# Performance work log

Hardware: AMD Instinct MI355X
Metric: run time of the kernel (lower is better)

## Reference

```python
import jax, jax.numpy as jnp
import numpy as np

EPS = 1e-5  # torch LayerNorm default


def setup_inputs() -> dict:
    key = jax.random.key(0)
    ks = jax.random.split(key, 6)
    B, C, H, W, D = 8, 128, 64, 64, 32
    x = jax.random.normal(ks[0], (B, C, H, W), dtype=jnp.float32)
    gamma = jnp.ones((C,), dtype=jnp.float32)
    beta = jnp.zeros((C,), dtype=jnp.float32)
    Wq = jax.random.normal(ks[1], (D, C), dtype=jnp.float32) * 0.02
    Wk = jax.random.normal(ks[2], (D, C), dtype=jnp.float32) * 0.02
    Wv = jax.random.normal(ks[3], (C, C), dtype=jnp.float32) * 0.02
    Wo = jax.random.normal(ks[4], (C, C), dtype=jnp.float32) * (1.0 / np.sqrt(C))
    bo = jnp.zeros((C,), dtype=jnp.float32)
    return {"x": x, "gamma": gamma, "beta": beta, "Wq": Wq, "Wk": Wk,
            "Wv": Wv, "Wo": Wo, "bo": bo}


def reference(x, gamma, beta, Wq, Wk, Wv, Wo, bo):
    B, C, H, W = x.shape
    # LayerNorm over channel dim (applied in NHWC in the original)
    xn = x.transpose(0, 2, 3, 1)                       # [B,H,W,C]
    mu = xn.mean(-1, keepdims=True)
    var = ((xn - mu) ** 2).mean(-1, keepdims=True)
    xn = (xn - mu) * jax.lax.rsqrt(var + EPS) * gamma + beta
    xn = xn.transpose(0, 3, 1, 2)                      # [B,C,H,W]
    # 1x1-conv projections == channel matmuls
    q = jnp.einsum('dc,bchw->bdhw', Wq, xn)
    k = jnp.einsum('dc,bchw->bdhw', Wk, xn)
    v = jnp.einsum('oc,bchw->bohw', Wv, xn)
    # full spatial attention: scores [B,H,W,H,W], softmax over key positions
    scores = jnp.einsum('bchw,bcxy->bhwxy', q, k)
    scores = scores.reshape(B, H, W, H * W)
    attn = jax.nn.softmax(scores, axis=-1).reshape(B, H, W, H, W)
    out = jnp.einsum('bhwxy,bcxy->bchw', attn, v)
    out = jnp.einsum('oc,bchw->bohw', Wo, out) + bo[None, :, None, None]
    return out + x
```

## Files before the change

kernel.cpp:

```cpp
#include <hip/hip_runtime.h>


#define NB 8
#define CCH 128
#define NTOK 4096
#define DQK 32
#define KT 64

typedef __attribute__((ext_vector_type(8))) short bf16x8;
typedef __attribute__((ext_vector_type(4))) float f32x4;
typedef unsigned short u16;
typedef unsigned int u32;

static __device__ __forceinline__ f32x4 mfma16(bf16x8 a, bf16x8 b, f32x4 c) {
  return __builtin_amdgcn_mfma_f32_16x16x32_bf16(a, b, c, 0, 0, 0);
}
static __device__ __forceinline__ u16 f2bf(float f) {
  union { float f; u32 u; } cv; cv.f = f;
  u32 u = cv.u;
  u += 0x7fffu + ((u >> 16) & 1u);
  return (u16)(u >> 16);
}
static __device__ __forceinline__ float bf2f(u16 v) {
  union { u32 u; float f; } cv; cv.u = ((u32)v) << 16;
  return cv.f;
}
static __device__ __forceinline__ u32 cvtpk(float lo, float hi) {
  u32 d;
  asm("v_cvt_pk_bf16_f32 %0, %1, %2" : "=v"(d) : "v"(lo), "v"(hi));
  return d;
}
static __device__ __forceinline__ void gload16(const void* g, void* l) {
  __builtin_amdgcn_global_load_lds(
      (const __attribute__((address_space(1))) void*)g,
      (__attribute__((address_space(3))) void*)l, 16, 0, 0);
}

__global__ __launch_bounds__(256) void wconv_kernel(
    const float* __restrict__ Wq, const float* __restrict__ Wk,
    const float* __restrict__ Wv, const float* __restrict__ Wo,
    u16* __restrict__ wcomb) {
  int idx = blockIdx.x * 256 + threadIdx.x;
  int r = idx >> 7;
  float v;
  if (r < 32)        v = Wq[idx];
  else if (r < 64)   v = Wk[idx - 4096];
  else if (r < 192)  v = Wv[idx - 8192];
  else               v = Wo[idx - 24576];
  wcomb[idx] = f2bf(v);
}

__global__ __launch_bounds__(256) void lnqkv_kernel(
    const float* __restrict__ x, const float* __restrict__ gamma,
    const float* __restrict__ beta, const u16* __restrict__ wcomb,
    u16* __restrict__ Qg, u16* __restrict__ Kg, u16* __restrict__ Vt) {
  __shared__ float tile[128][64];
  __shared__ float red[2][4][64];
  __shared__ u16   xt[64][130];
  int t = threadIdx.x;
  int lane = t & 63, cq = t >> 6;
  int b = blockIdx.x >> 6;
  int posb = (blockIdx.x & 63) << 6;
  const float* xb = x + ((size_t)b * CCH) * NTOK + posb;
  for (int i = 0; i < 32; ++i) {
    int c = cq * 32 + i;
    tile[c][lane] = xb[(size_t)c * NTOK + lane];
  }
  __syncthreads();
  float s = 0.f, s2 = 0.f;
  for (int i = 0; i < 32; ++i) {
    float v = tile[cq * 32 + i][lane];
    s += v; s2 += v * v;
  }
  red[0][cq][lane] = s; red[1][cq][lane] = s2;
  __syncthreads();
  float mu  = (red[0][0][lane] + red[0][1][lane] + red[0][2][lane] + red[0][3][lane]) * (1.f / 128.f);
  float ex2 = (red[1][0][lane] + red[1][1][lane] + red[1][2][lane] + red[1][3][lane]) * (1.f / 128.f);
  float rstd = rsqrtf(ex2 - mu * mu + 1e-5f);
  for (int i = 0; i < 32; ++i) {
    int c = cq * 32 + i;
    float v = (tile[c][lane] - mu) * rstd * gamma[c] + beta[c];
    xt[lane][c] = f2bf(v);
  }
  __syncthreads();
  int w = t >> 6, row16 = lane & 15, kgrp = lane >> 4;
  bf16x8 af[4];
  for (int ks = 0; ks < 4; ++ks)
    af[ks] = *(const bf16x8*)&xt[w * 16 + row16][ks * 32 + kgrp * 8];
  f32x4 zero = {0.f, 0.f, 0.f, 0.f};
  f32x4 acc[12];
  for (int nt = 0; nt < 12; ++nt) {
    acc[nt] = zero;
    for (int ks = 0; ks < 4; ++ks) {
      bf16x8 bf = *(const bf16x8*)&wcomb[(size_t)(nt * 16 + row16) * CCH + ks * 32 + kgrp * 8];
      acc[nt] = mfma16(af[ks], bf, acc[nt]);
    }
  }
  int tok0 = b * NTOK + posb;
  for (int nt = 0; nt < 12; ++nt) {
    int col = nt * 16 + row16;
    for (int r = 0; r < 4; ++r) {
      int token = tok0 + w * 16 + kgrp * 4 + r;
      if (col < 32) {
        Qg[(size_t)token * DQK + col] = f2bf(acc[nt][r] * 1.44269504f);
      } else if (col < 64) {
        Kg[(size_t)token * DQK + (col - 32)] = f2bf(acc[nt][r]);
      } else {
        int tl = token & (NTOK - 1);
        int kp = (tl & ~31) | ((tl & 12) << 1) | ((tl & 16) >> 2) | (tl & 3);
        Vt[((size_t)b * CCH + (col - 64)) * NTOK + kp] = f2bf(acc[nt][r]);
      }
    }
  }
}

template <int NS>
__global__ __launch_bounds__(256, 4) void attn_kernel(
    const u16* __restrict__ Qg, const u16* __restrict__ Kg,
    const u16* __restrict__ Vt, u16* __restrict__ Op,
    float* __restrict__ lp) {
  __shared__ u16 lds[2][10240];
  constexpr int KSEG = NTOK / NS;
  constexpr int NTILE = KSEG / KT;
  constexpr int BSH = (NS == 4) ? 7 : 6;
  int t = threadIdx.x;
  int w = t >> 6, lane = t & 63;
  int row16 = lane & 15, kgrp = lane >> 4;

  int cpx = (256 * NS) >> 3;
  int logical = (blockIdx.x & 7) * cpx + (blockIdx.x >> 3);
  int qblk = logical & 31;
  int part = (logical >> 5) & (NS - 1);
  int b = logical >> BSH;
  int q0 = qblk * 128;
  int kt0 = part * KSEG;

  const u16* Qb = Qg + ((size_t)(b * NTOK + q0 + w * 32)) * DQK;
  bf16x8 qf0 = *(const bf16x8*)&Qb[(size_t)row16 * DQK + kgrp * 8];
  bf16x8 qf1 = *(const bf16x8*)&Qb[(size_t)(16 + row16) * DQK + kgrp * 8];

  bf16x8 ones_b;
  {
    short one = (short)0x3F80;
    short val = (row16 == 0) ? one : (short)0;
    for (int j = 0; j < 8; ++j) ones_b[j] = val;
  }

  int pr = t >> 3, e8 = t & 7;
  int korig = e8 ^ (pr & 7);
  int kkey = pr * 2 + (korig >> 2);
  int kfs = korig & 3;
  const u16* ksrc = Kg + (size_t)(b * NTOK + kt0 + kkey) * DQK + kfs * 8;
  int cV = t >> 3;
  int sV = e8 ^ (cV & 7);
  const u16* vsrc = Vt + ((size_t)b * CCH + cV) * NTOK + kt0 + sV * 8;

  int kdst = w * 512;
  int vdst = w * 512;

  f32x4 zero = {0.f, 0.f, 0.f, 0.f};
  f32x4 o0[8], o1[8], ol0, ol1;
#pragma unroll
  for (int i = 0; i < 8; ++i) { o0[i] = zero; o1[i] = zero; }
  ol0 = zero; ol1 = zero;

  auto stage = [&](int bi, int tile) {
    const u16* kp_ = ksrc + (size_t)tile * (KT * DQK);
    gload16(kp_, &lds[bi][kdst]);
    const u16* vp_ = vsrc + tile * KT;
    gload16(vp_,          &lds[bi][2048 + vdst]);
    gload16(vp_ + 131072, &lds[bi][2048 + 2048 + vdst]);
    gload16(vp_ + 262144, &lds[bi][2048 + 4096 + vdst]);
    gload16(vp_ + 393216, &lds[bi][2048 + 6144 + vdst]);
  };

  auto compute = [&](int bi) {
    const u16* kb = &lds[bi][0];
    const u16* vb = &lds[bi][2048];
    f32x4 sa0[4], sa1[4];
#pragma unroll
    for (int nt = 0; nt < 4; ++nt) {
      int slot = (nt * 8 + (row16 >> 1)) * 8 +
                 ((((row16 & 1) << 2) + kgrp) ^ (row16 >> 1));
      bf16x8 kf = *(const bf16x8*)&kb[slot * 8];
      sa0[nt] = mfma16(kf, qf0, zero);
      sa1[nt] = mfma16(kf, qf1, zero);
    }
#pragma unroll
    for (int nt = 0; nt < 4; ++nt)
      for (int r = 0; r < 4; ++r) {
        sa0[nt][r] = __builtin_amdgcn_exp2f(sa0[nt][r]);
        sa1[nt][r] = __builtin_amdgcn_exp2f(sa1[nt][r]);
      }
    union PU { u32 d[4]; bf16x8 v; };
    PU pf0[2], pf1[2];
#pragma unroll
    for (int ks = 0; ks < 2; ++ks) {
      pf0[ks].d[0] = cvtpk(sa0[2 * ks][0], sa0[2 * ks][1]);
      pf0[ks].d[1] = cvtpk(sa0[2 * ks][2], sa0[2 * ks][3]);
      pf0[ks].d[2] = cvtpk(sa0[2 * ks + 1][0], sa0[2 * ks + 1][1]);
      pf0[ks].d[3] = cvtpk(sa0[2 * ks + 1][2], sa0[2 * ks + 1][3]);
      pf1[ks].d[0] = cvtpk(sa1[2 * ks][0], sa1[2 * ks][1]);
      pf1[ks].d[1] = cvtpk(sa1[2 * ks][2], sa1[2 * ks][3]);
      pf1[ks].d[2] = cvtpk(sa1[2 * ks + 1][0], sa1[2 * ks + 1][1]);
      pf1[ks].d[3] = cvtpk(sa1[2 * ks + 1][2], sa1[2 * ks + 1][3]);
    }
    ol0 = mfma16(pf0[0].v, ones_b, ol0);
    ol0 = mfma16(pf0[1].v, ones_b, ol0);
    ol1 = mfma16(pf1[0].v, ones_b, ol1);
    ol1 = mfma16(pf1[1].v, ones_b, ol1);
#pragma unroll
    for (int ks = 0; ks < 2; ++ks)
#pragma unroll
      for (int ntc = 0; ntc < 8; ++ntc) {
        int vslot = (ntc * 16 + row16) * 8 + (((ks << 2) + kgrp) ^ (row16 & 7));
        bf16x8 vf = *(const bf16x8*)&vb[vslot * 8];
        o0[ntc] = mfma16(pf0[ks].v, vf, o0[ntc]);
        o1[ntc] = mfma16(pf1[ks].v, vf, o1[ntc]);
      }
  };

  stage(0, 0);
  asm volatile("s_waitcnt vmcnt(0)" ::: "memory");
  __builtin_amdgcn_s_barrier();
  int cur = 0;
  for (int tile = 0; tile < NTILE - 1; ++tile) {
    stage(cur ^ 1, tile + 1);
    compute(cur);
    asm volatile("s_waitcnt vmcnt(0)" ::: "memory");
    __builtin_amdgcn_s_barrier();
    cur ^= 1;
  }
  compute(cur);

  u16* Opw = Op + (size_t)part * (32768 * CCH);
  int tokb = b * NTOK + q0 + w * 32;
#pragma unroll
  for (int r = 0; r < 4; ++r) {
    int tk0 = tokb + kgrp * 4 + r;
    int tk1 = tokb + 16 + kgrp * 4 + r;
#pragma unroll
    for (int ntc = 0; ntc < 8; ++ntc) {
      Opw[(size_t)tk0 * CCH + ntc * 16 + row16] = f2bf(o0[ntc][r]);
      Opw[(size_t)tk1 * CCH + ntc * 16 + row16] = f2bf(o1[ntc][r]);
    }
  }
  if (row16 == 0) {
#pragma unroll
    for (int r = 0; r < 4; ++r) {
      lp[part * 32768 + tokb + kgrp * 4 + r] = ol0[r];
      lp[part * 32768 + tokb + 16 + kgrp * 4 + r] = ol1[r];
    }
  }
}

__global__ __launch_bounds__(256) void out_kernel(
    const u16* __restrict__ Op, const float* __restrict__ lp, int ns,
    const u16* __restrict__ wcomb, const float* __restrict__ bo,
    const float* __restrict__ x, float* __restrict__ out) {
  int t = threadIdx.x;
  int w = t >> 6, lane = t & 63;
  int row16 = lane & 15, kgrp = lane >> 4;
  int tok0 = blockIdx.x * 64;
  int b = tok0 >> 12, tloc = tok0 & (NTOK - 1);
  int tokA = tok0 + w * 16 + row16;
  float lsum = 0.f;
  for (int j = 0; j < ns; ++j) lsum += lp[j * 32768 + tokA];
  float inv = 1.f / lsum;
  bf16x8 af[4];
  for (int ks = 0; ks < 4; ++ks) {
    float sum[8] = {0.f, 0.f, 0.f, 0.f, 0.f, 0.f, 0.f, 0.f};
    for (int j = 0; j < ns; ++j) {
      bf16x8 a = *(const bf16x8*)&Op[(size_t)j * (32768 * CCH) +
                                     (size_t)tokA * CCH + ks * 32 + kgrp * 8];
      for (int e = 0; e < 8; ++e) sum[e] += bf2f((u16)a[e]);
    }
    bf16x8 av;
    for (int e = 0; e < 8; ++e) av[e] = (short)f2bf(sum[e] * inv);
    af[ks] = av;
  }
  f32x4 zero = {0.f, 0.f, 0.f, 0.f};
  f32x4 acc[8];
  for (int nt = 0; nt < 8; ++nt) {
    acc[nt] = zero;
    for (int ks = 0; ks < 4; ++ks) {
      bf16x8 bf = *(const bf16x8*)&wcomb[(size_t)(192 + nt * 16 + row16) * CCH + ks * 32 + kgrp * 8];
      acc[nt] = mfma16(af[ks], bf, acc[nt]);
    }
  }
  for (int nt = 0; nt < 8; ++nt) {
    int cout = nt * 16 + row16;
    float bias = bo[cout];
    size_t base = ((size_t)b * CCH + cout) * NTOK + tloc + w * 16 + kgrp * 4;
    float4 xr = *(const float4*)&x[base];
    float4 ov;
    ov.x = acc[nt][0] + bias + xr.x;
    ov.y = acc[nt][1] + bias + xr.y;
    ov.z = acc[nt][2] + bias + xr.z;
    ov.w = acc[nt][3] + bias + xr.w;
    *(float4*)&out[base] = ov;
  }
}

extern "C" void kernel_launch(void* const* d_in, const int* in_sizes, int n_in,
                              void* d_out, int out_size, void* d_ws, size_t ws_size,
                              hipStream_t stream) {
  const float* x     = (const float*)d_in[0];
  const float* gamma = (const float*)d_in[1];
  const float* beta  = (const float*)d_in[2];
  const float* Wq    = (const float*)d_in[3];
  const float* Wk    = (const float*)d_in[4];
  const float* Wv    = (const float*)d_in[5];
  const float* Wo    = (const float*)d_in[6];
  const float* bo    = (const float*)d_in[7];
  float* out = (float*)d_out;

  unsigned char* ws = (unsigned char*)d_ws;
  u16* Qg    = (u16*)(ws);
  u16* Kg    = (u16*)(ws + 2097152);
  u16* Vt    = (u16*)(ws + 4194304);
  u16* wcomb = (u16*)(ws + 12582912);
  float* lp  = (float*)(ws + 12664832);
  u16* Op    = (u16*)(ws + 13189120);

  int ns = (ws_size >= 46743552u) ? 4 : 2;

  wconv_kernel<<<160, 256, 0, stream>>>(Wq, Wk, Wv, Wo, wcomb);
  lnqkv_kernel<<<512, 256, 0, stream>>>(x, gamma, beta, wcomb, Qg, Kg, Vt);
  if (ns == 4)
    attn_kernel<4><<<1024, 256, 0, stream>>>(Qg, Kg, Vt, Op, lp);
  else
    attn_kernel<2><<<512, 256, 0, stream>>>(Qg, Kg, Vt, Op, lp);
  out_kernel<<<512, 256, 0, stream>>>(Op, lp, ns, wcomb, bo, x, out);
}
```

Measured before the change: 93.34 us.

## Vectorize partial-output stores, prefetch K fragments, set MFMA priority, retile out kernel

The attention kernel now writes its bf16 partial outputs as packed 16-byte stores in the MFMA register layout instead of scattered 2-byte stores. It also prefetches the next tile's K fragments from LDS before the barrier, restructures the K staging loads, and raises wave priority around the MFMA block. The output kernel reads that packed layout, transposes it through LDS into MFMA A-fragments, and handles 128 tokens per block, so half as many blocks launch. The intent is to cut store and reload traffic. The cost is extra LDS use and a custom intermediate layout that both kernels must agree on.

New measurement: 113.8 us. 1.22x slower.

```diff
diff --git a/kernel.cpp b/kernel.cpp
--- a/kernel.cpp
+++ b/kernel.cpp
@@ -6,6 +6,7 @@
 #define NTOK 4096
 #define DQK 32
 #define KT 64
+#define PARTSZ 4194304
 
 typedef __attribute__((ext_vector_type(8))) short bf16x8;
 typedef __attribute__((ext_vector_type(4))) float f32x4;
@@ -141,21 +142,16 @@
 
   bf16x8 ones_b;
   {
-    short one = (short)0x3F80;
-    short val = (row16 == 0) ? one : (short)0;
+    short val = (row16 == 0) ? (short)0x3F80 : (short)0;
     for (int j = 0; j < 8; ++j) ones_b[j] = val;
   }
 
-  int pr = t >> 3, e8 = t & 7;
-  int korig = e8 ^ (pr & 7);
-  int kkey = pr * 2 + (korig >> 2);
-  int kfs = korig & 3;
-  const u16* ksrc = Kg + (size_t)(b * NTOK + kt0 + kkey) * DQK + kfs * 8;
+  int korig = (lane & 7) ^ (lane >> 3);
+  int kconst = (((lane >> 3) * 2 + (korig >> 2)) * 32) + (korig & 3) * 8;
+  const u16* ksrc = Kg + (size_t)(b * NTOK + kt0) * DQK + kconst;
   int cV = t >> 3;
-  int sV = e8 ^ (cV & 7);
+  int sV = (t & 7) ^ (cV & 7);
   const u16* vsrc = Vt + ((size_t)b * CCH + cV) * NTOK + kt0 + sV * 8;
-
-  int kdst = w * 512;
   int vdst = w * 512;
 
   f32x4 zero = {0.f, 0.f, 0.f, 0.f};
@@ -166,7 +162,9 @@
 
   auto stage = [&](int bi, int tile) {
     const u16* kp_ = ksrc + (size_t)tile * (KT * DQK);
-    gload16(kp_, &lds[bi][kdst]);
+#pragma unroll
+    for (int ii = 0; ii < 4; ++ii)
+      gload16(kp_ + ii * 512, &lds[bi][ii * 512]);
     const u16* vp_ = vsrc + tile * KT;
     gload16(vp_,          &lds[bi][2048 + vdst]);
     gload16(vp_ + 131072, &lds[bi][2048 + 2048 + vdst]);
@@ -174,17 +172,22 @@
     gload16(vp_ + 393216, &lds[bi][2048 + 6144 + vdst]);
   };
 
-  auto compute = [&](int bi) {
-    const u16* kb = &lds[bi][0];
-    const u16* vb = &lds[bi][2048];
-    f32x4 sa0[4], sa1[4];
+  auto loadK = [&](int bi, bf16x8* kf) {
 #pragma unroll
     for (int nt = 0; nt < 4; ++nt) {
       int slot = (nt * 8 + (row16 >> 1)) * 8 +
                  ((((row16 & 1) << 2) + kgrp) ^ (row16 >> 1));
-      bf16x8 kf = *(const bf16x8*)&kb[slot * 8];
-      sa0[nt] = mfma16(kf, qf0, zero);
-      sa1[nt] = mfma16(kf, qf1, zero);
+      kf[nt] = *(const bf16x8*)&lds[bi][slot * 8];
+    }
+  };
+
+  auto compute = [&](int bi, const bf16x8* kf) {
+    const u16* vb = &lds[bi][2048];
+    f32x4 sa0[4], sa1[4];
+#pragma unroll
+    for (int nt = 0; nt < 4; ++nt) {
+      sa0[nt] = mfma16(kf[nt], qf0, zero);
+      sa1[nt] = mfma16(kf[nt], qf1, zero);
     }
 #pragma unroll
     for (int nt = 0; nt < 4; ++nt)
@@ -205,6 +208,7 @@
       pf1[ks].d[2] = cvtpk(sa1[2 * ks + 1][0], sa1[2 * ks + 1][1]);
       pf1[ks].d[3] = cvtpk(sa1[2 * ks + 1][2], sa1[2 * ks + 1][3]);
     }
+    __builtin_amdgcn_s_setprio(1);
     ol0 = mfma16(pf0[0].v, ones_b, ol0);
     ol0 = mfma16(pf0[1].v, ones_b, ol0);
     ol1 = mfma16(pf1[0].v, ones_b, ol1);
@@ -218,33 +222,45 @@
         o0[ntc] = mfma16(pf0[ks].v, vf, o0[ntc]);
         o1[ntc] = mfma16(pf1[ks].v, vf, o1[ntc]);
       }
+    __builtin_amdgcn_s_setprio(0);
   };
 
+  bf16x8 kf[4];
   stage(0, 0);
   asm volatile("s_waitcnt vmcnt(0)" ::: "memory");
+  loadK(0, kf);
   __builtin_amdgcn_s_barrier();
   int cur = 0;
   for (int tile = 0; tile < NTILE - 1; ++tile) {
     stage(cur ^ 1, tile + 1);
-    compute(cur);
+    compute(cur, kf);
     asm volatile("s_waitcnt vmcnt(0)" ::: "memory");
+    loadK(cur ^ 1, kf);
     __builtin_amdgcn_s_barrier();
     cur ^= 1;
   }
-  compute(cur);
-
-  u16* Opw = Op + (size_t)part * (32768 * CCH);
+  compute(cur, kf);
+
+  u32 word[32];
+#pragma unroll
+  for (int sub = 0; sub < 2; ++sub) {
+#pragma unroll
+    for (int ntc = 0; ntc < 8; ++ntc) {
+      f32x4 ov = sub ? o1[ntc] : o0[ntc];
+      word[sub * 16 + ntc * 2]     = cvtpk(ov[0], ov[1]);
+      word[sub * 16 + ntc * 2 + 1] = cvtpk(ov[2], ov[3]);
+    }
+  }
+  u16* Opw = Op + (size_t)part * PARTSZ;
+  size_t blkb = ((size_t)(b * NTOK + q0)) * CCH;
+#pragma unroll
+  for (int j = 0; j < 8; ++j) {
+    uint4 v4;
+    v4.x = word[4 * j]; v4.y = word[4 * j + 1];
+    v4.z = word[4 * j + 2]; v4.w = word[4 * j + 3];
+    *(uint4*)&Opw[blkb + w * 4096 + j * 512 + lane * 8] = v4;
+  }
   int tokb = b * NTOK + q0 + w * 32;
-#pragma unroll
-  for (int r = 0; r < 4; ++r) {
-    int tk0 = tokb + kgrp * 4 + r;
-    int tk1 = tokb + 16 + kgrp * 4 + r;
-#pragma unroll
-    for (int ntc = 0; ntc < 8; ++ntc) {
-      Opw[(size_t)tk0 * CCH + ntc * 16 + row16] = f2bf(o0[ntc][r]);
-      Opw[(size_t)tk1 * CCH + ntc * 16 + row16] = f2bf(o1[ntc][r]);
-    }
-  }
   if (row16 == 0) {
 #pragma unroll
     for (int r = 0; r < 4; ++r) {
@@ -258,48 +274,87 @@
     const u16* __restrict__ Op, const float* __restrict__ lp, int ns,
     const u16* __restrict__ wcomb, const float* __restrict__ bo,
     const float* __restrict__ x, float* __restrict__ out) {
+  __shared__ float lred[128];
+  __shared__ u16 xt[128][132];
   int t = threadIdx.x;
   int w = t >> 6, lane = t & 63;
   int row16 = lane & 15, kgrp = lane >> 4;
-  int tok0 = blockIdx.x * 64;
+  int blk = blockIdx.x;
+  int tok0 = blk * 128;
   int b = tok0 >> 12, tloc = tok0 & (NTOK - 1);
-  int tokA = tok0 + w * 16 + row16;
-  float lsum = 0.f;
-  for (int j = 0; j < ns; ++j) lsum += lp[j * 32768 + tokA];
-  float inv = 1.f / lsum;
-  bf16x8 af[4];
+
+  if (t < 128) {
+    float s = 0.f;
+    for (int p = 0; p < ns; ++p) s += lp[p * 32768 + tok0 + t];
+    lred[t] = 1.f / s;
+  }
+  __syncthreads();
+  float linv[2][4];
+#pragma unroll
+  for (int sub = 0; sub < 2; ++sub)
+#pragma unroll
+    for (int r = 0; r < 4; ++r)
+      linv[sub][r] = lred[w * 32 + sub * 16 + kgrp * 4 + r];
+
+  size_t blkb = (size_t)tok0 * CCH;
+#pragma unroll
+  for (int j = 0; j < 8; ++j) {
+    float s[8] = {0.f, 0.f, 0.f, 0.f, 0.f, 0.f, 0.f, 0.f};
+    for (int p = 0; p < ns; ++p) {
+      uint4 v4 = *(const uint4*)&Op[(size_t)p * PARTSZ + blkb + w * 4096 + j * 512 + lane * 8];
+      u32 ww[4] = {v4.x, v4.y, v4.z, v4.w};
+#pragma unroll
+      for (int m = 0; m < 4; ++m) {
+        s[2 * m]     += bf2f((u16)(ww[m] & 0xffffu));
+        s[2 * m + 1] += bf2f((u16)(ww[m] >> 16));
+      }
+    }
+    int sub = j >> 2;
+#pragma unroll
+    for (int m = 0; m < 4; ++m) {
+      int i = 4 * j + m;
+      int ntc = (i >> 1) & 7, pr = i & 1;
+      int c = ntc * 16 + row16;
+#pragma unroll
+      for (int dd = 0; dd < 2; ++dd) {
+        int r = 2 * pr + dd;
+        xt[w * 32 + sub * 16 + kgrp * 4 + r][c] = f2bf(s[2 * m + dd] * linv[sub][r]);
+      }
+    }
+  }
+  __syncthreads();
+
+  f32x4 zero = {0.f, 0.f, 0.f, 0.f};
+  f32x4 acc[2][8];
+#pragma unroll
+  for (int sub = 0; sub < 2; ++sub)
+    for (int nt = 0; nt < 8; ++nt) acc[sub][nt] = zero;
+#pragma unroll
   for (int ks = 0; ks < 4; ++ks) {
-    float sum[8] = {0.f, 0.f, 0.f, 0.f, 0.f, 0.f, 0.f, 0.f};
-    for (int j = 0; j < ns; ++j) {
-      bf16x8 a = *(const bf16x8*)&Op[(size_t)j * (32768 * CCH) +
-                                     (size_t)tokA * CCH + ks * 32 + kgrp * 8];
-      for (int e = 0; e < 8; ++e) sum[e] += bf2f((u16)a[e]);
-    }
-    bf16x8 av;
-    for (int e = 0; e < 8; ++e) av[e] = (short)f2bf(sum[e] * inv);
-    af[ks] = av;
-  }
-  f32x4 zero = {0.f, 0.f, 0.f, 0.f};
-  f32x4 acc[8];
-  for (int nt = 0; nt < 8; ++nt) {
-    acc[nt] = zero;
-    for (int ks = 0; ks < 4; ++ks) {
-      bf16x8 bf = *(const bf16x8*)&wcomb[(size_t)(192 + nt * 16 + row16) * CCH + ks * 32 + kgrp * 8];
-      acc[nt] = mfma16(af[ks], bf, acc[nt]);
-    }
-  }
-  for (int nt = 0; nt < 8; ++nt) {
-    int cout = nt * 16 + row16;
-    float bias = bo[cout];
-    size_t base = ((size_t)b * CCH + cout) * NTOK + tloc + w * 16 + kgrp * 4;
-    float4 xr = *(const float4*)&x[base];
-    float4 ov;
-    ov.x = acc[nt][0] + bias + xr.x;
-    ov.y = acc[nt][1] + bias + xr.y;
-    ov.z = acc[nt][2] + bias + xr.z;
-    ov.w = acc[nt][3] + bias + xr.w;
-    *(float4*)&out[base] = ov;
-  }
+    bf16x8 af0 = *(const bf16x8*)&xt[w * 32 + row16][ks * 32 + kgrp * 8];
+    bf16x8 af1 = *(const bf16x8*)&xt[w * 32 + 16 + row16][ks * 32 + kgrp * 8];
+#pragma unroll
+    for (int nt = 0; nt < 8; ++nt) {
+      bf16x8 bfv = *(const bf16x8*)&wcomb[(size_t)(192 + nt * 16 + row16) * CCH + ks * 32 + kgrp * 8];
+      acc[0][nt] = mfma16(af0, bfv, acc[0][nt]);
+      acc[1][nt] = mfma16(af1, bfv, acc[1][nt]);
+    }
+  }
+#pragma unroll
+  for (int sub = 0; sub < 2; ++sub)
+#pragma unroll
+    for (int nt = 0; nt < 8; ++nt) {
+      int cout = nt * 16 + row16;
+      float bias = bo[cout];
+      size_t base = ((size_t)b * CCH + cout) * NTOK + tloc + w * 32 + sub * 16 + kgrp * 4;
+      float4 xr = *(const float4*)&x[base];
+      float4 ov;
+      ov.x = acc[sub][nt][0] + bias + xr.x;
+      ov.y = acc[sub][nt][1] + bias + xr.y;
+      ov.z = acc[sub][nt][2] + bias + xr.z;
+      ov.w = acc[sub][nt][3] + bias + xr.w;
+      *(float4*)&out[base] = ov;
+    }
 }
 
 extern "C" void kernel_launch(void* const* d_in, const int* in_sizes, int n_in,
@@ -331,5 +386,5 @@
     attn_kernel<4><<<1024, 256, 0, stream>>>(Qg, Kg, Vt, Op, lp);
   else
     attn_kernel<2><<<512, 256, 0, stream>>>(Qg, Kg, Vt, Op, lp);
-  out_kernel<<<512, 256, 0, stream>>>(Op, lp, ns, wcomb, bo, x, out);
-}
+  out_kernel<<<256, 256, 0, stream>>>(Op, lp, ns, wcomb, bo, x, out);
+}
```
